# Performance work log

Hardware: AMD Instinct MI355X
Metric: run time of the kernel (lower is better)

## Reference

```python
import jax, jax.numpy as jnp
import numpy as np

B, M, N = 16, 1024, 4096
CIN, HID = 67, 128  # in_channels+3, hid_channels
BN_EPS = 1e-5


def setup_inputs() -> dict:
    key = jax.random.key(0)
    ks = jax.random.split(key, 13)
    inp = {
        "cent_feat": jax.random.normal(ks[0], (B, M, CIN), dtype=jnp.float32),
        "feat": jax.random.normal(ks[1], (B, N, CIN), dtype=jnp.float32),
        "mask": jax.random.uniform(ks[2], (B, M, N), dtype=jnp.float32),
        # Conv1d(k=1, bias=False) weights, xavier-normal-ish scale
        "Wq": jax.random.normal(ks[3], (HID, CIN), dtype=jnp.float32) * np.float32(np.sqrt(2.0 / (HID + CIN))),
        "Wk": jax.random.normal(ks[4], (HID, CIN), dtype=jnp.float32) * np.float32(np.sqrt(2.0 / (HID + CIN))),
        # BatchNorm1d params (inference form)
        "gq": jax.random.uniform(ks[5], (HID,), dtype=jnp.float32, minval=0.5, maxval=1.5),
        "bq": jax.random.normal(ks[6], (HID,), dtype=jnp.float32) * 0.1,
        "mq": jax.random.normal(ks[7], (HID,), dtype=jnp.float32) * 0.1,
        "vq": jax.random.uniform(ks[8], (HID,), dtype=jnp.float32, minval=0.5, maxval=1.5),
        "gk": jax.random.uniform(ks[9], (HID,), dtype=jnp.float32, minval=0.5, maxval=1.5),
        "bk": jax.random.normal(ks[10], (HID,), dtype=jnp.float32) * 0.1,
        "mk": jax.random.normal(ks[11], (HID,), dtype=jnp.float32) * 0.1,
        "vk": jax.random.uniform(ks[12], (HID,), dtype=jnp.float32, minval=0.5, maxval=1.5),
    }
    return inp


def _bn(x, g, b, m, v):
    # BatchNorm1d over channel dim (last axis here), inference form
    return (x - m) * (g / jnp.sqrt(v + BN_EPS)) + b


def _l1_normalize(x, axis):
    # torch F.normalize(p=1): x / max(||x||_1, 1e-12)
    return x / jnp.maximum(jnp.sum(jnp.abs(x), axis=axis, keepdims=True), 1e-12)


def reference(cent_feat, feat, mask, Wq, Wk, gq, bq, mq, vq, gk, bk, mk, vk):
    # Conv1x1 (1x1 conv = channel matmul) + BN, no activation
    q = _bn(jnp.einsum("bmc,hc->bmh", cent_feat, Wq), gq, bq, mq, vq)  # [B,M,H]
    k = _bn(jnp.einsum("bnc,hc->bnh", feat, Wk), gk, bk, mk, vk)       # [B,N,H]
    adj = jnp.einsum("bmh,bnh->bmn", q, k)                              # [B,M,N]
    adj = jnp.where(mask < 1e-9, jnp.float32(-1e9), adj)
    adj = jax.nn.softmax(adj, axis=-1)
    adj = jnp.sqrt(mask + 1e-9) * jnp.sqrt(adj + 1e-9) - 1e-9
    adj = _l1_normalize(adj, axis=1)
    adj = _l1_normalize(adj, axis=-1)
    return adj
```

## Files before the change

kernel.cpp:

```cpp
#include <hip/hip_runtime.h>
#include <hip/hip_fp16.h>

#define B_ 16
#define M_ 1024
#define N_ 4096
#define H_ 128
#define CIN_ 67

typedef _Float16 half8 __attribute__((ext_vector_type(8)));
typedef _Float16 half4_t __attribute__((ext_vector_type(4)));
typedef float f32x4 __attribute__((ext_vector_type(4)));

#define SPA 104

__global__ __launch_bounds__(256) void k_embed(
    const float* __restrict__ cent, const float* __restrict__ feat,
    const float* __restrict__ Wq, const float* __restrict__ Wk,
    const float* __restrict__ gq, const float* __restrict__ bq,
    const float* __restrict__ mq, const float* __restrict__ vq,
    const float* __restrict__ gk, const float* __restrict__ bk,
    const float* __restrict__ mk, const float* __restrict__ vk,
    __half* __restrict__ q16, __half* __restrict__ k16)
{
  __shared__ __align__(16) __half al[128 * SPA];
  __shared__ __align__(16) __half wl[128 * SPA];
  __shared__ float scl[128], shl[128];

  const int tid = threadIdx.x;
  const int wg  = blockIdx.x;
  const bool isq = (wg < 128);
  const int row0 = isq ? wg * 128 : (wg - 128) * 128;
  const float* in = isq ? cent : feat;
  const float* W  = isq ? Wq : Wk;
  const float* g  = isq ? gq : gk;
  const float* bb = isq ? bq : bk;
  const float* mm = isq ? mq : mk;
  const float* vv = isq ? vq : vk;
  __half* outp = isq ? q16 : k16;

  for (int i = tid; i < 128 * 29; i += 256) {
    int r = i / 29, c = 67 + (i - r * 29);
    al[r * SPA + c] = __float2half(0.f);
    wl[r * SPA + c] = __float2half(0.f);
  }
  for (int i = tid; i < 128 * CIN_; i += 256) {
    int r = i / CIN_, c = i - r * CIN_;
    al[r * SPA + c] = __float2half(in[(size_t)row0 * CIN_ + i]);
    wl[r * SPA + c] = __float2half(W[i]);
  }
  if (tid < 128) {
    float s = g[tid] * rsqrtf(vv[tid] + 1e-5f);
    scl[tid] = s;
    shl[tid] = bb[tid] - mm[tid] * s;
  }
  __syncthreads();

  const int lane = tid & 63, wv = tid >> 6;
  const int col = lane & 15, quad = lane >> 4;

  f32x4 acc[2][8];
#pragma unroll
  for (int ms = 0; ms < 2; ++ms)
#pragma unroll
    for (int ns = 0; ns < 8; ++ns) acc[ms][ns] = (f32x4){0.f, 0.f, 0.f, 0.f};

#pragma unroll
  for (int kk = 0; kk < 3; ++kk) {
    half8 af[2], bf[8];
#pragma unroll
    for (int ms = 0; ms < 2; ++ms)
      af[ms] = *(const half8*)&al[(wv * 32 + ms * 16 + col) * SPA + kk * 32 + quad * 8];
#pragma unroll
    for (int ns = 0; ns < 8; ++ns)
      bf[ns] = *(const half8*)&wl[(ns * 16 + col) * SPA + kk * 32 + quad * 8];
#pragma unroll
    for (int ms = 0; ms < 2; ++ms)
#pragma unroll
      for (int ns = 0; ns < 8; ++ns)
        acc[ms][ns] = __builtin_amdgcn_mfma_f32_16x16x32_f16(af[ms], bf[ns], acc[ms][ns], 0, 0, 0);
  }

#pragma unroll
  for (int ms = 0; ms < 2; ++ms)
#pragma unroll
    for (int reg = 0; reg < 4; ++reg) {
      int r = wv * 32 + ms * 16 + quad * 4 + reg;
#pragma unroll
      for (int ns = 0; ns < 8; ++ns) {
        int h = ns * 16 + col;
        float v = acc[ms][ns][reg] * scl[h] + shl[h];
        outp[(size_t)(row0 + r) * H_ + h] = __float2half(v);
      }
    }
}

#define SPB 136

__global__ __launch_bounds__(256, 3) void k_attn1(
    const __half* __restrict__ q16, const __half* __restrict__ k16,
    float* __restrict__ Z)
{
  __shared__ __align__(16) __half ka[128 * SPB];

  const int tid = threadIdx.x;
  const int b = blockIdx.z, mt = blockIdx.y, ns = blockIdx.x;
  const int m0 = mt * 128;
  const int lane = tid & 63, wv = tid >> 6;
  const int col = lane & 15, quad = lane >> 4;

  const __half* kstrip = k16 + ((size_t)(b * N_) + ns * 512) * H_;

  uint4 kreg[8];
  {
    const uint4* srck0 = (const uint4*)kstrip;
#pragma unroll
    for (int j = 0; j < 8; ++j) kreg[j] = srck0[tid + 256 * j];
  }
  half8 qf[4][2];
  {
    const __half* qb = q16 + ((size_t)(b * M_) + m0 + wv * 32 + col) * H_;
#pragma unroll
    for (int kk = 0; kk < 4; ++kk)
#pragma unroll
      for (int ms = 0; ms < 2; ++ms)
        qf[kk][ms] = *(const half8*)(qb + (size_t)ms * 16 * H_ + kk * 32 + quad * 8);
  }

  float zacc[8];
#pragma unroll
  for (int i = 0; i < 8; ++i) zacc[i] = 0.f;

  for (int t = 0; t < 4; ++t) {
    if (t) __syncthreads();
#pragma unroll
    for (int j = 0; j < 8; ++j) {
      int i = tid + 256 * j;
      int r = i >> 4, c = i & 15;
      *(uint4*)&ka[r * SPB + c * 8] = kreg[j];
    }
    __syncthreads();
    if (t < 3) {
      const uint4* srck = (const uint4*)(kstrip + (size_t)(t + 1) * 128 * H_);
#pragma unroll
      for (int j = 0; j < 8; ++j) kreg[j] = srck[tid + 256 * j];
    }
    __builtin_amdgcn_sched_barrier(0);

    f32x4 acc[2][8];
#pragma unroll
    for (int ms = 0; ms < 2; ++ms)
#pragma unroll
      for (int nb = 0; nb < 8; ++nb) acc[ms][nb] = (f32x4){0.f, 0.f, 0.f, 0.f};

#pragma unroll
    for (int kk = 0; kk < 4; ++kk) {
#pragma unroll
      for (int nb = 0; nb < 8; ++nb) {
        half8 bf = *(const half8*)&ka[(nb * 16 + col) * SPB + kk * 32 + quad * 8];
        acc[0][nb] = __builtin_amdgcn_mfma_f32_16x16x32_f16(qf[kk][0], bf, acc[0][nb], 0, 0, 0);
        acc[1][nb] = __builtin_amdgcn_mfma_f32_16x16x32_f16(qf[kk][1], bf, acc[1][nb], 0, 0, 0);
      }
    }

#pragma unroll
    for (int ms = 0; ms < 2; ++ms)
#pragma unroll
      for (int reg = 0; reg < 4; ++reg) {
        float s = 0.f;
#pragma unroll
        for (int nb = 0; nb < 8; ++nb) s += __expf(acc[ms][nb][reg]);
        zacc[ms * 4 + reg] += s;
      }
  }

#pragma unroll
  for (int i = 0; i < 8; ++i) {
    zacc[i] += __shfl_xor(zacc[i], 1);
    zacc[i] += __shfl_xor(zacc[i], 2);
    zacc[i] += __shfl_xor(zacc[i], 4);
    zacc[i] += __shfl_xor(zacc[i], 8);
  }
  if (col == 0) {
#pragma unroll
    for (int i = 0; i < 8; ++i) {
      int m = m0 + wv * 32 + (i >> 2) * 16 + quad * 4 + (i & 3);
      atomicAdd(&Z[(size_t)b * M_ + m], zacc[i]);
    }
  }
}

__global__ __launch_bounds__(256, 3) void k_attn3(
    const __half* __restrict__ q16, const __half* __restrict__ k16,
    const float* __restrict__ mask, const float* __restrict__ Z,
    __half* __restrict__ t16, float* __restrict__ colsum)
{
  __shared__ __align__(16) __half qa[128 * SPB];

  const int tid = threadIdx.x;
  const int b = blockIdx.z, mt = blockIdx.y, nt = blockIdx.x;
  const int m0 = mt * 128, n0 = nt * 128;
  const int lane = tid & 63, wv = tid >> 6;
  const int col = lane & 15, quad = lane >> 4;

  uint4 qreg[8];
  {
    const uint4* srcq = (const uint4*)(q16 + ((size_t)(b * M_) + m0) * H_);
#pragma unroll
    for (int j = 0; j < 8; ++j) qreg[j] = srcq[tid + 256 * j];
  }
  half8 kf[4][2];
  {
    const __half* kb = k16 + ((size_t)(b * N_) + n0 + wv * 32 + col) * H_;
#pragma unroll
    for (int kk = 0; kk < 4; ++kk)
#pragma unroll
      for (int ms = 0; ms < 2; ++ms)
        kf[kk][ms] = *(const half8*)(kb + (size_t)ms * 16 * H_ + kk * 32 + quad * 8);
  }
  float zr[8];
#pragma unroll
  for (int nsm = 0; nsm < 8; ++nsm)
    zr[nsm] = Z[(size_t)b * M_ + m0 + nsm * 16 + col];
  float4 mv0[8];
  {
    const int nb = n0 + wv * 32 + quad * 4;
#pragma unroll
    for (int nsm = 0; nsm < 8; ++nsm)
      mv0[nsm] = *(const float4*)&mask[((size_t)b * M_ + m0 + nsm * 16 + col) * N_ + nb];
  }
  __builtin_amdgcn_sched_barrier(0);

#pragma unroll
  for (int j = 0; j < 8; ++j) {
    int i = tid + 256 * j;
    int r = i >> 4, c = i & 15;
    *(uint4*)&qa[r * SPB + c * 8] = qreg[j];
  }
  __syncthreads();

  f32x4 acc[2][8];
#pragma unroll
  for (int ms = 0; ms < 2; ++ms)
#pragma unroll
    for (int nb = 0; nb < 8; ++nb) acc[ms][nb] = (f32x4){0.f, 0.f, 0.f, 0.f};

#pragma unroll
  for (int kk = 0; kk < 4; ++kk) {
#pragma unroll
    for (int nb = 0; nb < 8; ++nb) {
      half8 bf = *(const half8*)&qa[(nb * 16 + col) * SPB + kk * 32 + quad * 8];
      acc[0][nb] = __builtin_amdgcn_mfma_f32_16x16x32_f16(kf[kk][0], bf, acc[0][nb], 0, 0, 0);
      acc[1][nb] = __builtin_amdgcn_mfma_f32_16x16x32_f16(kf[kk][1], bf, acc[1][nb], 0, 0, 0);
    }
  }

  float4 mv1[8];
  {
    const int nb = n0 + wv * 32 + 16 + quad * 4;
#pragma unroll
    for (int nsm = 0; nsm < 8; ++nsm)
      mv1[nsm] = *(const float4*)&mask[((size_t)b * M_ + m0 + nsm * 16 + col) * N_ + nb];
  }
  __builtin_amdgcn_sched_barrier(0);

#pragma unroll
  for (int i = 0; i < 8; ++i) zr[i] = __logf(zr[i]);

  float cs[8];
#pragma unroll
  for (int i = 0; i < 8; ++i) cs[i] = 0.f;

#define EPI(MSN, MV)                                                        \
  {                                                                         \
    const int nb = n0 + wv * 32 + (MSN) * 16 + quad * 4;                    \
    _Pragma("unroll")                                                       \
    for (int nsm = 0; nsm < 8; ++nsm) {                                     \
      const int m = m0 + nsm * 16 + col;                                    \
      const float lzv = zr[nsm];                                            \
      const size_t base = ((size_t)b * M_ + m) * N_ + nb;                   \
      const float4 mv = MV[nsm];                                            \
      half4_t h;                                                            \
      _Pragma("unroll")                                                     \
      for (int reg = 0; reg < 4; ++reg) {                                   \
        float mvv = (reg == 0) ? mv.x : (reg == 1) ? mv.y                   \
                  : (reg == 2) ? mv.z : mv.w;                               \
        float x = acc[MSN][nsm][reg];                                       \
        x = (mvv < 1e-9f) ? -1e9f : x;                                      \
        float p = __expf(x - lzv);                                          \
        float t = sqrtf((mvv + 1e-9f) * (p + 1e-9f)) - 1e-9f;               \
        h[reg] = (_Float16)t;                                               \
        cs[(MSN) * 4 + reg] += t;                                           \
      }                                                                     \
      *(half4_t*)&t16[base] = h;                                            \
    }                                                                       \
  }

  EPI(0, mv0)
  EPI(1, mv1)
#undef EPI

#pragma unroll
  for (int i = 0; i < 8; ++i) {
    cs[i] += __shfl_xor(cs[i], 1);
    cs[i] += __shfl_xor(cs[i], 2);
    cs[i] += __shfl_xor(cs[i], 4);
    cs[i] += __shfl_xor(cs[i], 8);
  }
  if (col == 0) {
#pragma unroll
    for (int i = 0; i < 8; ++i) {
      int n = n0 + wv * 32 + (i >> 2) * 16 + quad * 4 + (i & 3);
      atomicAdd(&colsum[(size_t)b * N_ + n], cs[i]);
    }
  }
}

__global__ __launch_bounds__(256) void k_icol(float* __restrict__ cs)
{
  int i = blockIdx.x * 256 + threadIdx.x;
  cs[i] = 1.f / fmaxf(cs[i], 1e-12f);
}

__global__ __launch_bounds__(256) void k_norm(
    const __half* __restrict__ t16, float* __restrict__ out,
    const float* __restrict__ icol)
{
  const int row = blockIdx.x;
  const int b = row >> 10;
  const half4_t* t4 = (const half4_t*)(t16 + (size_t)row * N_);
  float4* o4 = (float4*)(out + (size_t)row * N_);
  const float4* c4 = (const float4*)(icol + (size_t)b * N_);
  const int tid = threadIdx.x;

  float4 u[4];
  float s = 0.f;
#pragma unroll
  for (int j = 0; j < 4; ++j) {
    int idx = tid + 256 * j;
    half4_t h = t4[idx];
    float4 c = c4[idx];
    u[j].x = (float)h[0] * c.x;
    u[j].y = (float)h[1] * c.y;
    u[j].z = (float)h[2] * c.z;
    u[j].w = (float)h[3] * c.w;
    s += u[j].x + u[j].y + u[j].z + u[j].w;
  }
  s += __shfl_xor(s, 1);
  s += __shfl_xor(s, 2);
  s += __shfl_xor(s, 4);
  s += __shfl_xor(s, 8);
  s += __shfl_xor(s, 16);
  s += __shfl_xor(s, 32);
  __shared__ float red[4];
  if ((tid & 63) == 0) red[tid >> 6] = s;
  __syncthreads();
  float tot = red[0] + red[1] + red[2] + red[3];
  float inv = 1.f / fmaxf(tot, 1e-12f);
#pragma unroll
  for (int j = 0; j < 4; ++j) {
    int idx = tid + 256 * j;
    float4 v = u[j];
    v.x *= inv; v.y *= inv; v.z *= inv; v.w *= inv;
    o4[idx] = v;
  }
}

extern "C" void kernel_launch(void* const* d_in, const int* in_sizes, int n_in,
                              void* d_out, int out_size, void* d_ws, size_t ws_size,
                              hipStream_t stream) {
  const float* cent = (const float*)d_in[0];
  const float* feat = (const float*)d_in[1];
  const float* mask = (const float*)d_in[2];
  const float* Wq = (const float*)d_in[3];
  const float* Wk = (const float*)d_in[4];
  const float* gq = (const float*)d_in[5];
  const float* bq = (const float*)d_in[6];
  const float* mq = (const float*)d_in[7];
  const float* vq = (const float*)d_in[8];
  const float* gk = (const float*)d_in[9];
  const float* bk = (const float*)d_in[10];
  const float* mk = (const float*)d_in[11];
  const float* vk = (const float*)d_in[12];
  float* out = (float*)d_out;

  char* ws = (char*)d_ws;
  __half* q16  = (__half*)(ws + 0);
  __half* k16  = (__half*)(ws + 4194304);
  __half* t16  = (__half*)(ws + 20971520);
  float* colsum= (float*)(ws + 155189248);
  float* Zr    = (float*)(ws + 155451392);

  hipMemsetAsync(colsum, 0, 262144 + 65536, stream);

  k_embed<<<640, 256, 0, stream>>>(cent, feat, Wq, Wk, gq, bq, mq, vq,
                                   gk, bk, mk, vk, q16, k16);

  dim3 g1(8, 8, 16);
  k_attn1<<<g1, 256, 0, stream>>>(q16, k16, Zr);

  dim3 g3(N_ / 128, M_ / 128, B_);
  k_attn3<<<g3, 256, 0, stream>>>(q16, k16, mask, Zr, t16, colsum);
  k_icol<<<B_ * N_ / 256, 256, 0, stream>>>(colsum);
  k_norm<<<B_ * M_, 256, 0, stream>>>(t16, out, colsum);
}
```

Baseline: 638.4 us.

## Fold log2e into q scale, split k staging, stage output via LDS

Folds log2(e) into the q BatchNorm scale and shift so both attention kernels can use exp2f and log2f instead of natural exp and log. In k_attn1, the next K tile is now loaded in two halves interleaved with the per-half exp sums, which cuts the registers held for prefetch. In k_attn3, mask loads move into the epilogue instead of being prefetched early, and the fp16 output tile is staged through LDS so global writes become coalesced 16-byte rows. Occupancy hints rise from 3 to 4 blocks per CU. The trade-off is less latency hiding for the mask loads and extra barriers and LDS traffic.

After: 618.4 us. 1.03x faster.

```diff
diff --git a/kernel.cpp b/kernel.cpp
--- a/kernel.cpp
+++ b/kernel.cpp
@@ -50,8 +50,9 @@
   }
   if (tid < 128) {
     float s = g[tid] * rsqrtf(vv[tid] + 1e-5f);
-    scl[tid] = s;
-    shl[tid] = bb[tid] - mm[tid] * s;
+    float sc = isq ? 1.44269504088896f : 1.f;
+    scl[tid] = s * sc;
+    shl[tid] = (bb[tid] - mm[tid] * s) * sc;
   }
   __syncthreads();
 
@@ -96,7 +97,7 @@
 
 #define SPB 136
 
-__global__ __launch_bounds__(256, 3) void k_attn1(
+__global__ __launch_bounds__(256, 4) void k_attn1(
     const __half* __restrict__ q16, const __half* __restrict__ k16,
     float* __restrict__ Z)
 {
@@ -110,11 +111,16 @@
 
   const __half* kstrip = k16 + ((size_t)(b * N_) + ns * 512) * H_;
 
-  uint4 kreg[8];
   {
-    const uint4* srck0 = (const uint4*)kstrip;
-#pragma unroll
-    for (int j = 0; j < 8; ++j) kreg[j] = srck0[tid + 256 * j];
+    uint4 kr[8];
+    const uint4* s0 = (const uint4*)kstrip;
+#pragma unroll
+    for (int j = 0; j < 8; ++j) kr[j] = s0[tid + 256 * j];
+#pragma unroll
+    for (int j = 0; j < 8; ++j) {
+      int i = tid + 256 * j;
+      *(uint4*)&ka[(i >> 4) * SPB + (i & 15) * 8] = kr[j];
+    }
   }
   half8 qf[4][2];
   {
@@ -125,27 +131,13 @@
       for (int ms = 0; ms < 2; ++ms)
         qf[kk][ms] = *(const half8*)(qb + (size_t)ms * 16 * H_ + kk * 32 + quad * 8);
   }
+  __syncthreads();
 
   float zacc[8];
 #pragma unroll
   for (int i = 0; i < 8; ++i) zacc[i] = 0.f;
 
   for (int t = 0; t < 4; ++t) {
-    if (t) __syncthreads();
-#pragma unroll
-    for (int j = 0; j < 8; ++j) {
-      int i = tid + 256 * j;
-      int r = i >> 4, c = i & 15;
-      *(uint4*)&ka[r * SPB + c * 8] = kreg[j];
-    }
-    __syncthreads();
-    if (t < 3) {
-      const uint4* srck = (const uint4*)(kstrip + (size_t)(t + 1) * 128 * H_);
-#pragma unroll
-      for (int j = 0; j < 8; ++j) kreg[j] = srck[tid + 256 * j];
-    }
-    __builtin_amdgcn_sched_barrier(0);
-
     f32x4 acc[2][8];
 #pragma unroll
     for (int ms = 0; ms < 2; ++ms)
@@ -162,15 +154,48 @@
       }
     }
 
-#pragma unroll
-    for (int ms = 0; ms < 2; ++ms)
-#pragma unroll
-      for (int reg = 0; reg < 4; ++reg) {
-        float s = 0.f;
-#pragma unroll
-        for (int nb = 0; nb < 8; ++nb) s += __expf(acc[ms][nb][reg]);
-        zacc[ms * 4 + reg] += s;
+    const uint4* sn = (const uint4*)(kstrip + (size_t)(t + 1) * 128 * H_);
+    uint4 kr2[4];
+    if (t < 3) {
+      __syncthreads();
+#pragma unroll
+      for (int j = 0; j < 4; ++j) kr2[j] = sn[tid + 256 * j];
+    }
+
+#pragma unroll
+    for (int reg = 0; reg < 4; ++reg) {
+      float s = 0.f;
+#pragma unroll
+      for (int nb = 0; nb < 8; ++nb) s += exp2f(acc[0][nb][reg]);
+      zacc[reg] += s;
+    }
+
+    if (t < 3) {
+#pragma unroll
+      for (int j = 0; j < 4; ++j) {
+        int i = tid + 256 * j;
+        *(uint4*)&ka[(i >> 4) * SPB + (i & 15) * 8] = kr2[j];
       }
+#pragma unroll
+      for (int j = 0; j < 4; ++j) kr2[j] = sn[tid + 256 * (j + 4)];
+    }
+
+#pragma unroll
+    for (int reg = 0; reg < 4; ++reg) {
+      float s = 0.f;
+#pragma unroll
+      for (int nb = 0; nb < 8; ++nb) s += exp2f(acc[1][nb][reg]);
+      zacc[4 + reg] += s;
+    }
+
+    if (t < 3) {
+#pragma unroll
+      for (int j = 0; j < 4; ++j) {
+        int i = tid + 256 * (j + 4);
+        *(uint4*)&ka[(i >> 4) * SPB + (i & 15) * 8] = kr2[j];
+      }
+      __syncthreads();
+    }
   }
 
 #pragma unroll
@@ -189,7 +214,7 @@
   }
 }
 
-__global__ __launch_bounds__(256, 3) void k_attn3(
+__global__ __launch_bounds__(256, 4) void k_attn3(
     const __half* __restrict__ q16, const __half* __restrict__ k16,
     const float* __restrict__ mask, const float* __restrict__ Z,
     __half* __restrict__ t16, float* __restrict__ colsum)
@@ -202,11 +227,16 @@
   const int lane = tid & 63, wv = tid >> 6;
   const int col = lane & 15, quad = lane >> 4;
 
-  uint4 qreg[8];
   {
-    const uint4* srcq = (const uint4*)(q16 + ((size_t)(b * M_) + m0) * H_);
-#pragma unroll
-    for (int j = 0; j < 8; ++j) qreg[j] = srcq[tid + 256 * j];
+    uint4 qr[8];
+    const uint4* sq = (const uint4*)(q16 + ((size_t)(b * M_) + m0) * H_);
+#pragma unroll
+    for (int j = 0; j < 8; ++j) qr[j] = sq[tid + 256 * j];
+#pragma unroll
+    for (int j = 0; j < 8; ++j) {
+      int i = tid + 256 * j;
+      *(uint4*)&qa[(i >> 4) * SPB + (i & 15) * 8] = qr[j];
+    }
   }
   half8 kf[4][2];
   {
@@ -216,25 +246,6 @@
 #pragma unroll
       for (int ms = 0; ms < 2; ++ms)
         kf[kk][ms] = *(const half8*)(kb + (size_t)ms * 16 * H_ + kk * 32 + quad * 8);
-  }
-  float zr[8];
-#pragma unroll
-  for (int nsm = 0; nsm < 8; ++nsm)
-    zr[nsm] = Z[(size_t)b * M_ + m0 + nsm * 16 + col];
-  float4 mv0[8];
-  {
-    const int nb = n0 + wv * 32 + quad * 4;
-#pragma unroll
-    for (int nsm = 0; nsm < 8; ++nsm)
-      mv0[nsm] = *(const float4*)&mask[((size_t)b * M_ + m0 + nsm * 16 + col) * N_ + nb];
-  }
-  __builtin_amdgcn_sched_barrier(0);
-
-#pragma unroll
-  for (int j = 0; j < 8; ++j) {
-    int i = tid + 256 * j;
-    int r = i >> 4, c = i & 15;
-    *(uint4*)&qa[r * SPB + c * 8] = qreg[j];
   }
   __syncthreads();
 
@@ -253,51 +264,48 @@
       acc[1][nb] = __builtin_amdgcn_mfma_f32_16x16x32_f16(kf[kk][1], bf, acc[1][nb], 0, 0, 0);
     }
   }
-
-  float4 mv1[8];
-  {
-    const int nb = n0 + wv * 32 + 16 + quad * 4;
-#pragma unroll
-    for (int nsm = 0; nsm < 8; ++nsm)
-      mv1[nsm] = *(const float4*)&mask[((size_t)b * M_ + m0 + nsm * 16 + col) * N_ + nb];
-  }
-  __builtin_amdgcn_sched_barrier(0);
-
-#pragma unroll
-  for (int i = 0; i < 8; ++i) zr[i] = __logf(zr[i]);
+  __syncthreads();
+
+  float lz[8];
+#pragma unroll
+  for (int nsm = 0; nsm < 8; ++nsm)
+    lz[nsm] = __log2f(Z[(size_t)b * M_ + m0 + nsm * 16 + col]);
 
   float cs[8];
 #pragma unroll
   for (int i = 0; i < 8; ++i) cs[i] = 0.f;
 
-#define EPI(MSN, MV)                                                        \
-  {                                                                         \
-    const int nb = n0 + wv * 32 + (MSN) * 16 + quad * 4;                    \
-    _Pragma("unroll")                                                       \
-    for (int nsm = 0; nsm < 8; ++nsm) {                                     \
-      const int m = m0 + nsm * 16 + col;                                    \
-      const float lzv = zr[nsm];                                            \
-      const size_t base = ((size_t)b * M_ + m) * N_ + nb;                   \
-      const float4 mv = MV[nsm];                                            \
-      half4_t h;                                                            \
-      _Pragma("unroll")                                                     \
-      for (int reg = 0; reg < 4; ++reg) {                                   \
-        float mvv = (reg == 0) ? mv.x : (reg == 1) ? mv.y                   \
-                  : (reg == 2) ? mv.z : mv.w;                               \
-        float x = acc[MSN][nsm][reg];                                       \
-        x = (mvv < 1e-9f) ? -1e9f : x;                                      \
-        float p = __expf(x - lzv);                                          \
-        float t = sqrtf((mvv + 1e-9f) * (p + 1e-9f)) - 1e-9f;               \
-        h[reg] = (_Float16)t;                                               \
-        cs[(MSN) * 4 + reg] += t;                                           \
-      }                                                                     \
-      *(half4_t*)&t16[base] = h;                                            \
-    }                                                                       \
-  }
-
-  EPI(0, mv0)
-  EPI(1, mv1)
-#undef EPI
+#pragma unroll
+  for (int msN = 0; msN < 2; ++msN) {
+    const int nl = wv * 32 + msN * 16 + quad * 4;
+#pragma unroll
+    for (int nsm = 0; nsm < 8; ++nsm) {
+      const int ml = nsm * 16 + col;
+      const float lzv = lz[nsm];
+      const float4 mv = *(const float4*)&mask[((size_t)b * M_ + m0 + ml) * N_ + n0 + nl];
+      half4_t h;
+#pragma unroll
+      for (int reg = 0; reg < 4; ++reg) {
+        float mvv = (reg == 0) ? mv.x : (reg == 1) ? mv.y : (reg == 2) ? mv.z : mv.w;
+        float x = acc[msN][nsm][reg];
+        x = (mvv < 1e-9f) ? -1e9f : x;
+        float p = exp2f(x - lzv);
+        float t = sqrtf((mvv + 1e-9f) * (p + 1e-9f)) - 1e-9f;
+        h[reg] = (_Float16)t;
+        cs[msN * 4 + reg] += t;
+      }
+      *(half4_t*)&qa[ml * SPB + nl] = h;
+    }
+  }
+  __syncthreads();
+
+#pragma unroll
+  for (int j = 0; j < 8; ++j) {
+    int i = tid + 256 * j;
+    int r = i >> 4, u = i & 15;
+    *(uint4*)&t16[((size_t)(b * M_) + m0 + r) * N_ + n0 + u * 8] =
+        *(const uint4*)&qa[r * SPB + u * 8];
+  }
 
 #pragma unroll
   for (int i = 0; i < 8; ++i) {
```
